# Performance work log

Measured on AMD Instinct MI355X. Metric: run time of the kernel, lower is better.

Reference implementation:

```python
import jax, jax.numpy as jnp
import numpy as np

B, S, D, H = 2, 2048, 1024, 16
DK = D // H


def setup_inputs() -> dict:
    key = jax.random.key(0)
    ks = jax.random.split(key, 7)
    x = jax.random.normal(ks[0], (B, S, D), dtype=jnp.float32)
    gamma = jax.random.normal(ks[1], (D,), dtype=jnp.float32)
    mask = jax.random.randint(ks[2], (B, S), 0, 2, dtype=jnp.int32)
    w_qkv_w = jax.random.normal(ks[3], (D, 3 * D), dtype=jnp.float32) / np.sqrt(D)
    w_qkv_b = jax.random.normal(ks[4], (3 * D,), dtype=jnp.float32) * 0.02
    w_o_w = jax.random.normal(ks[5], (D, D), dtype=jnp.float32) / np.sqrt(D)
    w_o_b = jax.random.normal(ks[6], (D,), dtype=jnp.float32) * 0.02
    return {"x": x, "gamma": gamma, "mask": mask, "w_qkv_w": w_qkv_w,
            "w_qkv_b": w_qkv_b, "w_o_w": w_o_w, "w_o_b": w_o_b}


def reference(x, gamma, mask, w_qkv_w, w_qkv_b, w_o_w, w_o_b):
    b, s, d = x.shape
    # QKV projection, then per-head interleaved chunk (matches torch view+chunk)
    qkv = x @ w_qkv_w + w_qkv_b                      # [B,S,3D]
    qkv = qkv.reshape(b, s, H, 3 * DK).transpose(0, 2, 1, 3)  # [B,H,S,3*dk]
    q, k, v = jnp.split(qkv, 3, axis=-1)             # each [B,H,S,dk]
    scale = 1.0 / np.sqrt(DK).astype(np.float32)
    scores = jnp.einsum('bhqd,bhkd->bhqk', q, k) * scale  # [B,H,S,S]
    m = mask[:, None, None, :]                       # 2D mask -> [B,1,1,S]
    scores = jnp.where(m == 0, -jnp.inf, scores)
    attn = jax.nn.softmax(scores, axis=-1)           # dropout p=0.0 -> identity
    out = jnp.einsum('bhqk,bhkd->bhqd', attn, v)     # [B,H,S,dk]
    out = out.transpose(0, 2, 1, 3).reshape(b, s, d) # [B,S,D]
    out = out @ w_o_w + w_o_b
    return (gamma + 1.0) * out
```

## Files before the change

kernel.cpp:

```cpp
#include <hip/hip_runtime.h>
#include <hip/hip_bf16.h>


using bf16 = __hip_bfloat16;
typedef __attribute__((ext_vector_type(8))) short bf16x8;
typedef __attribute__((ext_vector_type(4))) float f32x4;

#define QSCALE 0.18033688011112042f

static __device__ __forceinline__ f32x4 mfma_bf16(bf16x8 a, bf16x8 b, f32x4 c) {
    return __builtin_amdgcn_mfma_f32_16x16x32_bf16(a, b, c, 0, 0, 0);
}

static __device__ __forceinline__ void gld_lds16(const void* g, void* s) {
    __builtin_amdgcn_global_load_lds(
        (const __attribute__((address_space(1))) unsigned int*)g,
        (__attribute__((address_space(3))) unsigned int*)s,
        16, 0, 0);
}

static __device__ __forceinline__ unsigned int pk_bf16(float lo, float hi) {
    unsigned int ul = __builtin_bit_cast(unsigned int, lo) + 0x8000u;
    unsigned int uh = __builtin_bit_cast(unsigned int, hi) + 0x8000u;
    return __builtin_amdgcn_perm(uh, ul, 0x07060302u);
}

__global__ void prep_kernel(const float* __restrict__ x, bf16* __restrict__ xb,
                            const float* __restrict__ wqkv, bf16* __restrict__ wqkvT,
                            const float* __restrict__ wo, bf16* __restrict__ woT) {
    __shared__ float tile[32][33];
    int blk = blockIdx.x;
    if (blk < 4096) {
        int i = blk * 256 + threadIdx.x;
        float4 f = reinterpret_cast<const float4*>(x)[i];
        xb[4*i+0] = __float2bfloat16(f.x);
        xb[4*i+1] = __float2bfloat16(f.y);
        xb[4*i+2] = __float2bfloat16(f.z);
        xb[4*i+3] = __float2bfloat16(f.w);
        return;
    }
    int xo = threadIdx.x & 31, yo = threadIdx.x >> 5;
    if (blk < 7168) {
        int idx = blk - 4096;
        int c0 = (idx % 96) * 32, r0 = (idx / 96) * 32;
#pragma unroll
        for (int i = 0; i < 32; i += 8)
            tile[yo + i][xo] = wqkv[(size_t)(r0 + yo + i) * 3072 + c0 + xo];
        __syncthreads();
#pragma unroll
        for (int i = 0; i < 32; i += 8) {
            int c = c0 + yo + i;
            int hh = c / 192, rem = c - hh * 192;
            int which = rem >> 6, dk = rem & 63;
            int rowp = which * 1024 + hh * 64 + dk;
            float sc = (which == 0) ? QSCALE : 1.0f;
            wqkvT[(size_t)rowp * 1024 + r0 + xo] = __float2bfloat16(tile[xo][yo + i] * sc);
        }
    } else {
        int idx = blk - 7168;
        int c0 = (idx & 31) * 32, r0 = (idx >> 5) * 32;
#pragma unroll
        for (int i = 0; i < 32; i += 8)
            tile[yo + i][xo] = wo[(size_t)(r0 + yo + i) * 1024 + c0 + xo];
        __syncthreads();
#pragma unroll
        for (int i = 0; i < 32; i += 8)
            woT[(size_t)(c0 + yo + i) * 1024 + r0 + xo] = __float2bfloat16(tile[xo][yo + i]);
    }
}

template <int EPI, int TM, int MINW>
__global__ __launch_bounds__(256, MINW)
void gemm_bt_kernel(const bf16* __restrict__ A, const bf16* __restrict__ Bt,
                    int M, int N, int K,
                    const float* __restrict__ bias, const float* __restrict__ gamma,
                    bf16* __restrict__ Qout, bf16* __restrict__ Kout, bf16* __restrict__ Vout,
                    float* __restrict__ Cout) {
    constexpr int MI = TM / 32;
    constexpr int CA = TM / 32;
    __shared__ __align__(16) bf16 smem[TM * 64 + 128 * 64];
    bf16* As = smem;
    bf16* Bs = smem + TM * 64;

    const int tid  = threadIdx.x;
    const int wave = tid >> 6, lane = tid & 63;
    const int quad = lane >> 4, l16 = lane & 15;
    const int wr = wave >> 1, wc = wave & 1;
    const int bm = blockIdx.y, bn = blockIdx.x;

    f32x4 acc[MI][4] = {};

    const int crow = lane >> 3;
    const int sblk = (lane & 7) ^ (crow & 7);
    const bf16* gA[CA]; const bf16* gB[4]; bf16* lA[CA]; bf16* lB[4];
#pragma unroll
    for (int c = 0; c < CA; ++c) {
        int ch = wave * CA + c;
        gA[c] = A + (size_t)(bm * TM + ch * 8 + crow) * K + sblk * 8;
        lA[c] = As + ch * 512 + lane * 8;
    }
#pragma unroll
    for (int c = 0; c < 4; ++c) {
        int ch = wave * 4 + c;
        gB[c] = Bt + (size_t)(bn * 128 + ch * 8 + crow) * K + sblk * 8;
        lB[c] = Bs + ch * 512 + lane * 8;
    }
    const int xr = l16 & 7;

    for (int k0 = 0; k0 < K; k0 += 64) {
#pragma unroll
        for (int c = 0; c < CA; ++c) gld_lds16(gA[c] + k0, lA[c]);
#pragma unroll
        for (int c = 0; c < 4; ++c) gld_lds16(gB[c] + k0, lB[c]);
        __syncthreads();
#pragma unroll
        for (int ks = 0; ks < 2; ++ks) {
            bf16x8 af[MI], bfr[4];
#pragma unroll
            for (int mi = 0; mi < MI; ++mi)
                af[mi] = *(const bf16x8*)(As + (wr * (TM/2) + mi * 16 + l16) * 64 + ((4 * ks + quad) ^ xr) * 8);
#pragma unroll
            for (int ni = 0; ni < 4; ++ni)
                bfr[ni] = *(const bf16x8*)(Bs + (wc * 64 + ni * 16 + l16) * 64 + ((4 * ks + quad) ^ xr) * 8);
#pragma unroll
            for (int mi = 0; mi < MI; ++mi)
#pragma unroll
                for (int ni = 0; ni < 4; ++ni)
                    acc[mi][ni] = mfma_bf16(af[mi], bfr[ni], acc[mi][ni]);
        }
        __syncthreads();
    }

    if (EPI == 0 && bn >= 16) {
        __syncthreads();
        uint2* Tu = (uint2*)smem;
#pragma unroll
        for (int mi = 0; mi < MI; ++mi) {
#pragma unroll
            for (int ni = 0; ni < 4; ++ni) {
                int colL = wc * 64 + ni * 16 + l16;
                float bv = bias[(2 * (bn - 16) + wc) * 192 + 128 + (ni * 16 + l16)];
                uint2 pk;
                pk.x = pk_bf16(acc[mi][ni][0] + bv, acc[mi][ni][1] + bv);
                pk.y = pk_bf16(acc[mi][ni][2] + bv, acc[mi][ni][3] + bv);
                int rg = wr * 16 + mi * 4 + quad;
                Tu[colL * 32 + (rg ^ (colL & 31))] = pk;
            }
        }
        __syncthreads();
        const int sub = tid & 15, rbase = tid >> 4;
        const int cs = sub >> 3, aa = (sub >> 2) & 1, qq = sub & 3;
        const int g1 = cs * 16 + aa * 8 + qq;
        const int g2 = g1 + 4;
        const int b = bm >> 4;
        const int s0 = (bm & 15) * 128;
#pragma unroll
        for (int j = 0; j < 8; ++j) {
            int rt = rbase + 16 * j;
            int hh = 2 * (bn - 16) + (rt >> 6), dk = rt & 63;
            uint2 lo = Tu[rt * 32 + (g1 ^ (rt & 31))];
            uint2 hi = Tu[rt * 32 + (g2 ^ (rt & 31))];
            uint4 val; val.x = lo.x; val.y = lo.y; val.z = hi.x; val.w = hi.y;
            *(uint4*)(Vout + (((size_t)b * 16 + hh) * 64 + dk) * 2048 + s0 + sub * 8) = val;
        }
        return;
    }

#pragma unroll
    for (int mi = 0; mi < MI; ++mi) {
#pragma unroll
        for (int ni = 0; ni < 4; ++ni) {
            int col = bn * 128 + wc * 64 + ni * 16 + l16;
            if (EPI == 0) {
                int which = col >> 10, hh = (col >> 6) & 15, dk = col & 63;
                float bv = bias[hh * 192 + which * 64 + dk];
                if (which == 0) bv *= QSCALE;
                bf16* dst = which ? Kout : Qout;
#pragma unroll
                for (int r = 0; r < 4; ++r) {
                    int row = bm * TM + wr * (TM/2) + mi * 16 + quad * 4 + r;
                    int b = row >> 11, s = row & 2047;
                    dst[(((size_t)b * 16 + hh) * 2048 + s) * 64 + dk] =
                        __float2bfloat16(acc[mi][ni][r] + bv);
                }
            } else {
                float g1 = gamma[col] + 1.0f, bv = bias[col];
#pragma unroll
                for (int r = 0; r < 4; ++r) {
                    int row = bm * TM + wr * (TM/2) + mi * 16 + quad * 4 + r;
                    Cout[(size_t)row * N + col] = g1 * (acc[mi][ni][r] + bv);
                }
            }
        }
    }
}

__global__ __launch_bounds__(128, 1)
void attn_kernel(const bf16* __restrict__ Qb, const bf16* __restrict__ Kb,
                 const bf16* __restrict__ Vtp, const int* __restrict__ mask,
                 bf16* __restrict__ Aout) {
    __shared__ __align__(16) bf16 Ks[2][64 * 64];
    __shared__ __align__(16) bf16 Vs[2][64 * 64];
    __shared__ float Biass[2][64];

    const int bh = blockIdx.y;
    const int b = bh >> 4, h = bh & 15;
    const int q0 = blockIdx.x * 128;
    const int tid = threadIdx.x;
    const int wave = tid >> 6, lane = tid & 63;
    const int quad = lane >> 4, l16 = lane & 15;
    const int xr = l16 & 7;

    bf16x8 aq[4][2];
#pragma unroll
    for (int m = 0; m < 4; ++m) {
        const bf16* qp = Qb + ((size_t)bh * 2048 + q0 + wave * 64 + m * 16 + l16) * 64;
        aq[m][0] = *(const bf16x8*)(qp + quad * 8);
        aq[m][1] = *(const bf16x8*)(qp + 32 + quad * 8);
    }

    bf16x8 ones;
#pragma unroll
    for (int j = 0; j < 8; ++j) ones[j] = (short)0x3F80;

    f32x4 O[4][4] = {};
    f32x4 Lacc[4] = {};

    const int r8 = lane >> 3, b8 = lane & 7;
    const int srcb = b8 ^ r8;
    const bf16* gK = Kb  + ((size_t)bh * 2048 + wave * 8 + r8) * 64 + srcb * 8;
    const bf16* gV = Vtp + ((size_t)bh * 64 + wave * 8 + r8) * 2048 + srcb * 8;
    bf16* lK[2][4]; bf16* lV[2][4];
#pragma unroll
    for (int p = 0; p < 2; ++p)
#pragma unroll
        for (int c = 0; c < 4; ++c) {
            lK[p][c] = Ks[p] + c * 1024 + wave * 512 + lane * 8;
            lV[p][c] = Vs[p] + c * 1024 + wave * 512 + lane * 8;
        }

    int mreg = 0;
#pragma unroll
    for (int c = 0; c < 4; ++c) {
        gld_lds16(gK + c * 1024, lK[0][c]);
        gld_lds16(gV + (size_t)c * 32768, lV[0][c]);
    }
    if (tid < 64) {
        Biass[0][tid] = mask[b * 2048 + tid] ? -24.0f : -1e30f;
        mreg = mask[b * 2048 + 64 + tid];
    }

    for (int kt = 0; kt < 32; ++kt) {
        __syncthreads();
        const int cur = kt & 1, nxt = cur ^ 1;

        if (kt + 1 < 32) {
#pragma unroll
            for (int c = 0; c < 4; ++c) {
                gld_lds16(gK + (size_t)(kt + 1) * 4096 + c * 1024, lK[nxt][c]);
                gld_lds16(gV + (kt + 1) * 64 + (size_t)c * 32768, lV[nxt][c]);
            }
            if (tid < 64) Biass[nxt][tid] = mreg ? -24.0f : -1e30f;
        }
        if (kt + 2 < 32 && tid < 64) mreg = mask[b * 2048 + (kt + 2) * 64 + tid];

        f32x4 bias4[4];
        bf16x8 bk[4][2];
#pragma unroll
        for (int kt4 = 0; kt4 < 4; ++kt4) {
            bias4[kt4] = *(const f32x4*)(&Biass[cur][0] + kt4 * 16 + quad * 4);
            const bf16* kp = Ks[cur] + (kt4 * 16 + l16) * 64;
            bk[kt4][0] = *(const bf16x8*)(kp + (quad ^ xr) * 8);
            bk[kt4][1] = *(const bf16x8*)(kp + ((quad + 4) ^ xr) * 8);
        }
        bf16x8 bv8[2][4];
#pragma unroll
        for (int a = 0; a < 2; ++a)
#pragma unroll
            for (int nt = 0; nt < 4; ++nt)
                bv8[a][nt] = *(const bf16x8*)(Vs[cur] + (nt * 16 + l16) * 64 + ((a * 4 + quad) ^ xr) * 8);

#pragma unroll
        for (int m = 0; m < 4; ++m) {
            f32x4 sv[4];
#pragma unroll
            for (int kt4 = 0; kt4 < 4; ++kt4) {
                f32x4 c = {0.f, 0.f, 0.f, 0.f};
                c = mfma_bf16(bk[kt4][0], aq[m][0], c);
                c = mfma_bf16(bk[kt4][1], aq[m][1], c);
                sv[kt4] = c;
            }
            float p[4][4];
#pragma unroll
            for (int kt4 = 0; kt4 < 4; ++kt4)
#pragma unroll
                for (int r = 0; r < 4; ++r)
                    p[kt4][r] = __builtin_amdgcn_exp2f(sv[kt4][r] + bias4[kt4][r]);

#pragma unroll
            for (int a = 0; a < 2; ++a) {
                uint4 uv;
                uv.x = pk_bf16(p[2*a][0],   p[2*a][1]);
                uv.y = pk_bf16(p[2*a][2],   p[2*a][3]);
                uv.z = pk_bf16(p[2*a+1][0], p[2*a+1][1]);
                uv.w = pk_bf16(p[2*a+1][2], p[2*a+1][3]);
                bf16x8 pa = __builtin_bit_cast(bf16x8, uv);
                Lacc[m] = mfma_bf16(pa, ones, Lacc[m]);
#pragma unroll
                for (int nt = 0; nt < 4; ++nt)
                    O[m][nt] = mfma_bf16(pa, bv8[a][nt], O[m][nt]);
            }
        }
    }

#pragma unroll
    for (int m = 0; m < 4; ++m) {
        float inv[4];
#pragma unroll
        for (int r = 0; r < 4; ++r) inv[r] = __builtin_amdgcn_rcpf(Lacc[m][r]);
#pragma unroll
        for (int nt = 0; nt < 4; ++nt) {
#pragma unroll
            for (int r = 0; r < 4; ++r) {
                int row = q0 + wave * 64 + m * 16 + quad * 4 + r;
                Aout[((size_t)b * 2048 + row) * 1024 + h * 64 + nt * 16 + l16] =
                    __float2bfloat16(O[m][nt][r] * inv[r]);
            }
        }
    }
}

extern "C" void kernel_launch(void* const* d_in, const int* in_sizes, int n_in,
                              void* d_out, int out_size, void* d_ws, size_t ws_size,
                              hipStream_t stream) {
    const float* x     = (const float*)d_in[0];
    const float* gamma = (const float*)d_in[1];
    const int*   mask  = (const int*)d_in[2];
    const float* wqkv  = (const float*)d_in[3];
    const float* bqkv  = (const float*)d_in[4];
    const float* wo    = (const float*)d_in[5];
    const float* bo    = (const float*)d_in[6];
    float* out = (float*)d_out;

    char* ws = (char*)d_ws;
    const size_t MB = 1u << 20;
    bf16* xb    = (bf16*)(ws);
    bf16* wqkvT = (bf16*)(ws + 8 * MB);
    bf16* woT   = (bf16*)(ws + 14 * MB);
    bf16* Qb    = (bf16*)(ws + 16 * MB);
    bf16* Kb    = (bf16*)(ws + 24 * MB);
    bf16* Vt    = (bf16*)(ws + 32 * MB);
    bf16* attn  = (bf16*)(ws + 40 * MB);

    prep_kernel<<<8192, 256, 0, stream>>>(x, xb, wqkv, wqkvT, wo, woT);

    gemm_bt_kernel<0, 128, 3><<<dim3(24, 32), 256, 0, stream>>>(
        xb, wqkvT, 4096, 3072, 1024, bqkv, nullptr, Qb, Kb, Vt, nullptr);

    attn_kernel<<<dim3(16, 32), 128, 0, stream>>>(Qb, Kb, Vt, mask, attn);

    gemm_bt_kernel<1, 64, 4><<<dim3(8, 64), 256, 0, stream>>>(
        attn, woT, 4096, 1024, 1024, bo, gamma, nullptr, nullptr, nullptr, out);
}
```

Baseline: 191.9 us.

## Load K/V tiles directly from global into registers with double-buffered prefetch

The attention kernel no longer stages K, V and mask tiles through LDS with async global-to-LDS copies and block barriers. Each wave now loads its MFMA operand fragments straight from global memory into registers, ping-ponging between two register sets so the next tile is prefetched while the current one is computed. This removes the LDS traffic and the __syncthreads. In exchange both waves load K/V redundantly from global/L2, register pressure roughly doubles for operands, and the per-lane loads are strided rather than coalesced. The last iteration also does a wasted reload of tile 0.

```diff
diff --git a/kernel.cpp b/kernel.cpp
--- a/kernel.cpp
+++ b/kernel.cpp
@@ -199,17 +199,12 @@
 void attn_kernel(const bf16* __restrict__ Qb, const bf16* __restrict__ Kb,
                  const bf16* __restrict__ Vtp, const int* __restrict__ mask,
                  bf16* __restrict__ Aout) {
-    __shared__ __align__(16) bf16 Ks[2][64 * 64];
-    __shared__ __align__(16) bf16 Vs[2][64 * 64];
-    __shared__ float Biass[2][64];
-
     const int bh = blockIdx.y;
     const int b = bh >> 4, h = bh & 15;
     const int q0 = blockIdx.x * 128;
     const int tid = threadIdx.x;
     const int wave = tid >> 6, lane = tid & 63;
     const int quad = lane >> 4, l16 = lane & 15;
-    const int xr = l16 & 7;
 
     bf16x8 aq[4][2];
 #pragma unroll
@@ -226,60 +221,37 @@
     f32x4 O[4][4] = {};
     f32x4 Lacc[4] = {};
 
-    const int r8 = lane >> 3, b8 = lane & 7;
-    const int srcb = b8 ^ r8;
-    const bf16* gK = Kb  + ((size_t)bh * 2048 + wave * 8 + r8) * 64 + srcb * 8;
-    const bf16* gV = Vtp + ((size_t)bh * 64 + wave * 8 + r8) * 2048 + srcb * 8;
-    bf16* lK[2][4]; bf16* lV[2][4];
-#pragma unroll
-    for (int p = 0; p < 2; ++p)
-#pragma unroll
-        for (int c = 0; c < 4; ++c) {
-            lK[p][c] = Ks[p] + c * 1024 + wave * 512 + lane * 8;
-            lV[p][c] = Vs[p] + c * 1024 + wave * 512 + lane * 8;
-        }
-
-    int mreg = 0;
-#pragma unroll
-    for (int c = 0; c < 4; ++c) {
-        gld_lds16(gK + c * 1024, lK[0][c]);
-        gld_lds16(gV + (size_t)c * 32768, lV[0][c]);
-    }
-    if (tid < 64) {
-        Biass[0][tid] = mask[b * 2048 + tid] ? -24.0f : -1e30f;
-        mreg = mask[b * 2048 + 64 + tid];
-    }
-
-    for (int kt = 0; kt < 32; ++kt) {
-        __syncthreads();
-        const int cur = kt & 1, nxt = cur ^ 1;
-
-        if (kt + 1 < 32) {
-#pragma unroll
-            for (int c = 0; c < 4; ++c) {
-                gld_lds16(gK + (size_t)(kt + 1) * 4096 + c * 1024, lK[nxt][c]);
-                gld_lds16(gV + (kt + 1) * 64 + (size_t)c * 32768, lV[nxt][c]);
-            }
-            if (tid < 64) Biass[nxt][tid] = mreg ? -24.0f : -1e30f;
-        }
-        if (kt + 2 < 32 && tid < 64) mreg = mask[b * 2048 + (kt + 2) * 64 + tid];
-
+    const bf16* kbase = Kb  + ((size_t)bh * 2048 + l16) * 64 + quad * 8;
+    const bf16* vbase = Vtp + ((size_t)bh * 64 + l16) * 2048 + quad * 8;
+    const int*  mbase = mask + b * 2048 + quad * 4;
+
+    bf16x8 bkA[4][2], bvA[2][4]; int4 mA[4];
+    bf16x8 bkB[4][2], bvB[2][4]; int4 mB[4];
+
+    auto loadT = [&](int kt, bf16x8 bk[4][2], bf16x8 bv[2][4], int4 mq[4]) {
+#pragma unroll
+        for (int kt4 = 0; kt4 < 4; ++kt4) {
+            const bf16* p = kbase + (size_t)(kt * 64 + kt4 * 16) * 64;
+            bk[kt4][0] = *(const bf16x8*)p;
+            bk[kt4][1] = *(const bf16x8*)(p + 32);
+            mq[kt4] = *(const int4*)(mbase + kt * 64 + kt4 * 16);
+        }
+#pragma unroll
+        for (int a = 0; a < 2; ++a)
+#pragma unroll
+            for (int nt = 0; nt < 4; ++nt)
+                bv[a][nt] = *(const bf16x8*)(vbase + (size_t)nt * 32768 + kt * 64 + a * 32);
+    };
+
+    auto step = [&](bf16x8 bk[4][2], bf16x8 bv[2][4], int4 mq[4]) {
         f32x4 bias4[4];
-        bf16x8 bk[4][2];
 #pragma unroll
         for (int kt4 = 0; kt4 < 4; ++kt4) {
-            bias4[kt4] = *(const f32x4*)(&Biass[cur][0] + kt4 * 16 + quad * 4);
-            const bf16* kp = Ks[cur] + (kt4 * 16 + l16) * 64;
-            bk[kt4][0] = *(const bf16x8*)(kp + (quad ^ xr) * 8);
-            bk[kt4][1] = *(const bf16x8*)(kp + ((quad + 4) ^ xr) * 8);
-        }
-        bf16x8 bv8[2][4];
-#pragma unroll
-        for (int a = 0; a < 2; ++a)
-#pragma unroll
-            for (int nt = 0; nt < 4; ++nt)
-                bv8[a][nt] = *(const bf16x8*)(Vs[cur] + (nt * 16 + l16) * 64 + ((a * 4 + quad) ^ xr) * 8);
-
+            bias4[kt4][0] = mq[kt4].x ? -24.0f : -1e30f;
+            bias4[kt4][1] = mq[kt4].y ? -24.0f : -1e30f;
+            bias4[kt4][2] = mq[kt4].z ? -24.0f : -1e30f;
+            bias4[kt4][3] = mq[kt4].w ? -24.0f : -1e30f;
+        }
 #pragma unroll
         for (int m = 0; m < 4; ++m) {
             f32x4 sv[4];
@@ -308,9 +280,18 @@
                 Lacc[m] = mfma_bf16(pa, ones, Lacc[m]);
 #pragma unroll
                 for (int nt = 0; nt < 4; ++nt)
-                    O[m][nt] = mfma_bf16(pa, bv8[a][nt], O[m][nt]);
-            }
-        }
+                    O[m][nt] = mfma_bf16(pa, bv[a][nt], O[m][nt]);
+            }
+        }
+    };
+
+    loadT(0, bkA, bvA, mA);
+    for (int kt = 0; kt < 32; kt += 2) {
+        loadT(kt + 1, bkB, bvB, mB);
+        step(bkA, bvA, mA);
+        int n2 = (kt + 2 < 32) ? kt + 2 : 0;
+        loadT(n2, bkA, bvA, mA);
+        step(bkB, bvB, mB);
     }
 
 #pragma unroll
```

Result: slower. 203.1 us (+5.9%).
